# Performance work log

Measured on AMD Instinct MI355X. Metric: run time of the kernel, lower is better.

The kernel has to match this reference:

```python
import jax, jax.numpy as jnp
import numpy as np

N_NODES = 100000
N_EDGES = 600000
IN_FEATS = 128
OUT_FEATS = 128
BN_EPS = 1e-5


def setup_inputs() -> dict:
    key = jax.random.key(0)
    ks = jax.random.split(key, 8)
    x = jax.random.normal(ks[0], (N_NODES, IN_FEATS), dtype=jnp.float32)
    edge_index = jax.random.randint(ks[1], (2, N_EDGES), 0, N_NODES, dtype=jnp.int64)
    # GCNConv linear weight (no bias in lin), bias added after aggregation
    W = jax.random.normal(ks[2], (IN_FEATS, OUT_FEATS), dtype=jnp.float32) / np.sqrt(IN_FEATS)
    b = jax.random.normal(ks[3], (OUT_FEATS,), dtype=jnp.float32) * 0.01
    # BatchNorm affine params
    gamma = jnp.ones((OUT_FEATS,), dtype=jnp.float32)
    beta = jnp.zeros((OUT_FEATS,), dtype=jnp.float32)
    # residual Linear: y = x @ W_res + b_res (W_res stored [in, out])
    W_res = jax.random.normal(ks[4], (IN_FEATS, OUT_FEATS), dtype=jnp.float32) / np.sqrt(IN_FEATS)
    b_res = jax.random.normal(ks[5], (OUT_FEATS,), dtype=jnp.float32) * 0.01
    return {"x": x, "edge_index": edge_index, "W": W, "b": b,
            "gamma": gamma, "beta": beta, "W_res": W_res, "b_res": b_res}


def _gcn_forward(x, edge_index, W, b, gamma, beta, W_res, b_res):
    n = x.shape[0]
    # --- GCNConv (PyG defaults): add self-loops, symmetric normalization ---
    loops = jnp.arange(n, dtype=edge_index.dtype)
    row = jnp.concatenate([edge_index[0], loops])  # source nodes
    col = jnp.concatenate([edge_index[1], loops])  # destination nodes
    deg = jax.ops.segment_sum(jnp.ones_like(col, dtype=x.dtype), col, num_segments=n)
    dinv = jax.lax.rsqrt(deg)  # deg >= 1 thanks to self-loops
    norm = dinv[row] * dinv[col]  # [E+N]
    h = x @ W  # [N, out]
    msg = h[row] * norm[:, None]  # gather + scale, [E+N, out]
    agg = jax.ops.segment_sum(msg, col, num_segments=n) + b  # scatter-add + bias
    # --- ReLU + BatchNorm (training mode, biased variance) ---
    r = jax.nn.relu(agg)
    mean = jnp.mean(r, axis=0)
    var = jnp.mean(jnp.square(r - mean), axis=0)
    bn = gamma * (r - mean) * jax.lax.rsqrt(var + BN_EPS) + beta
    # --- residual dense path ---
    res = x @ W_res + b_res
    return bn + res


def reference(x, edge_index, W, b, gamma, beta, W_res, b_res):
    return _gcn_forward(x, edge_index, W, b, gamma, beta, W_res, b_res)
```

## Files before the change

kernel.cpp:

```cpp
#include <hip/hip_runtime.h>

#define NN 100000
#define NE 600000
#define F  128
#define BN_EPS 1e-5f


__global__ void k_detect(const unsigned* __restrict__ ei, int* __restrict__ flag)
{
    __shared__ int any;
    if (threadIdx.x == 0) any = 0;
    __syncthreads();
    unsigned v = ei[2 * threadIdx.x + 1];
    if (v != 0u) atomicOr(&any, 1);
    __syncthreads();
    if (threadIdx.x == 0) *flag = (any == 0) ? 1 : 0;
}

__global__ void k_init(int* __restrict__ cnt, float* __restrict__ colsum, float* __restrict__ colsq)
{
    int i = blockIdx.x * 256 + threadIdx.x;
    if (i <= NN) cnt[i] = 0;
    if (i < F) { colsum[i] = 0.f; colsq[i] = 0.f; }
}

__global__ void k_count(const void* __restrict__ ei, const int* __restrict__ flag, int* __restrict__ cnt)
{
    int e = blockIdx.x * 256 + threadIdx.x;
    if (e >= NE) return;
    int col;
    if (*flag) col = (int)((const long long*)ei)[NE + e];
    else       col = ((const int*)ei)[NE + e];
    atomicAdd(&cnt[col], 1);
}

__global__ void k_dinv(const int* __restrict__ cnt, float* __restrict__ dinv)
{
    int i = blockIdx.x * 256 + threadIdx.x;
    if (i < NN) {
        float d = (float)(cnt[i] + 1);
        float r = rsqrtf(d);
        r = r * (1.5f - 0.5f * d * r * r);
        dinv[i] = r;
    }
}

__global__ void k_bsum(const int* __restrict__ cnt, int* __restrict__ bsum)
{
    __shared__ int s[256];
    int b = blockIdx.x, t = threadIdx.x;
    int i = b * 256 + t;
    s[t] = (i <= NN) ? cnt[i] : 0;
    __syncthreads();
    for (int o = 128; o > 0; o >>= 1) {
        if (t < o) s[t] += s[t + o];
        __syncthreads();
    }
    if (t == 0) bsum[b] = s[0];
}

__global__ void k_bscan(const int* __restrict__ bsum, int* __restrict__ bbase)
{
    __shared__ int s[512];
    int t = threadIdx.x;
    int v = (t < 391) ? bsum[t] : 0;
    s[t] = v;
    __syncthreads();
    for (int o = 1; o < 512; o <<= 1) {
        int tmp = (t >= o) ? s[t - o] : 0;
        __syncthreads();
        s[t] += tmp;
        __syncthreads();
    }
    if (t < 391) bbase[t] = s[t] - v;
}

__global__ void k_offsets(const int* __restrict__ cnt, const int* __restrict__ bbase,
                          int* __restrict__ off, int* __restrict__ cur)
{
    __shared__ int s[256];
    int b = blockIdx.x, t = threadIdx.x;
    int i = b * 256 + t;
    int v = (i <= NN) ? cnt[i] : 0;
    s[t] = v;
    __syncthreads();
    for (int o = 1; o < 256; o <<= 1) {
        int tmp = (t >= o) ? s[t - o] : 0;
        __syncthreads();
        s[t] += tmp;
        __syncthreads();
    }
    int excl = s[t] - v + bbase[b];
    if (i <= NN) {
        off[i] = excl;
        if (i < NN) cur[i] = excl;
    }
}

__global__ void k_place(const void* __restrict__ ei, const int* __restrict__ flag,
                        int* __restrict__ cur, int* __restrict__ csr)
{
    int e = blockIdx.x * 256 + threadIdx.x;
    if (e >= NE) return;
    int row, col;
    if (*flag) {
        row = (int)((const long long*)ei)[e];
        col = (int)((const long long*)ei)[NE + e];
    } else {
        row = ((const int*)ei)[e];
        col = ((const int*)ei)[NE + e];
    }
    int slot = atomicAdd(&cur[col], 1);
    csr[slot] = row;
}

__global__ __launch_bounds__(256) void k_agg(const float* __restrict__ x, const float* __restrict__ dinv,
                                             const int* __restrict__ off, const int* __restrict__ csr,
                                             float* __restrict__ aggx)
{
    int g = threadIdx.x >> 5;
    int lane = threadIdx.x & 31;
    int node = blockIdx.x * 8 + g;
    if (node >= NN) return;
    float di = dinv[node];
    float4 v = ((const float4*)(x + (size_t)node * F))[lane];
    float4 acc;
    acc.x = v.x * di; acc.y = v.y * di; acc.z = v.z * di; acc.w = v.w * di;
    int e0 = off[node], e1 = off[node + 1];
    for (int e = e0; e < e1; ++e) {
        int row = csr[e];
        float s = dinv[row];
        float4 u = ((const float4*)(x + (size_t)row * F))[lane];
        acc.x = fmaf(u.x, s, acc.x);
        acc.y = fmaf(u.y, s, acc.y);
        acc.z = fmaf(u.z, s, acc.z);
        acc.w = fmaf(u.w, s, acc.w);
    }
    float4 o;
    o.x = acc.x * di; o.y = acc.y * di; o.z = acc.z * di; o.w = acc.w * di;
    ((float4*)(aggx + (size_t)node * F))[lane] = o;
}

__global__ __launch_bounds__(256, 2) void k_gemm(
    float* __restrict__ A, const float* __restrict__ X,
    const float* __restrict__ W, const float* __restrict__ Wr,
    const float* __restrict__ bias, const float* __restrict__ biasr,
    float* __restrict__ res_out, float* __restrict__ colsum, float* __restrict__ colsq)
{
    __shared__ float At[64][F];
    __shared__ float Xt[64][F];
    __shared__ float Wa[16][F];
    __shared__ float Wb[16][F];

    const int tid = threadIdx.x;
    const int tx = tid & 31;
    const int ty = tid >> 5;
    const int r0 = blockIdx.x * 64;

#pragma unroll
    for (int it = 0; it < 8; ++it) {
        int idx = tid + it * 256;
        int row = idx >> 5;
        int k4 = (idx & 31) << 2;
        int gr = r0 + row;
        float4 va = make_float4(0.f, 0.f, 0.f, 0.f);
        float4 vx = va;
        if (gr < NN) {
            va = *(const float4*)(A + (size_t)gr * F + k4);
            vx = *(const float4*)(X + (size_t)gr * F + k4);
        }
        *(float4*)(&At[row][k4]) = va;
        *(float4*)(&Xt[row][k4]) = vx;
    }

    float acc1[8][4], acc2[8][4];
#pragma unroll
    for (int i = 0; i < 8; ++i)
#pragma unroll
        for (int j = 0; j < 4; ++j) { acc1[i][j] = 0.f; acc2[i][j] = 0.f; }

    for (int c = 0; c < 8; ++c) {
        __syncthreads();
#pragma unroll
        for (int it = 0; it < 2; ++it) {
            int idx = tid + it * 256;
            int kr = idx >> 5;
            int kc = (idx & 31) << 2;
            *(float4*)(&Wa[kr][kc]) = *(const float4*)(W  + (c * 16 + kr) * F + kc);
            *(float4*)(&Wb[kr][kc]) = *(const float4*)(Wr + (c * 16 + kr) * F + kc);
        }
        __syncthreads();
#pragma unroll
        for (int k0 = 0; k0 < 16; k0 += 4) {
            float w1[4][4], w2[4][4];
#pragma unroll
            for (int kk = 0; kk < 4; ++kk) {
                float4 t1 = *(const float4*)(&Wa[k0 + kk][tx * 4]);
                float4 t2 = *(const float4*)(&Wb[k0 + kk][tx * 4]);
                w1[kk][0] = t1.x; w1[kk][1] = t1.y; w1[kk][2] = t1.z; w1[kk][3] = t1.w;
                w2[kk][0] = t2.x; w2[kk][1] = t2.y; w2[kk][2] = t2.z; w2[kk][3] = t2.w;
            }
#pragma unroll
            for (int i = 0; i < 8; ++i) {
                float4 a4 = *(const float4*)(&At[ty * 8 + i][c * 16 + k0]);
                float4 x4 = *(const float4*)(&Xt[ty * 8 + i][c * 16 + k0]);
                float av[4] = {a4.x, a4.y, a4.z, a4.w};
                float xv[4] = {x4.x, x4.y, x4.z, x4.w};
#pragma unroll
                for (int kk = 0; kk < 4; ++kk)
#pragma unroll
                    for (int j = 0; j < 4; ++j) {
                        acc1[i][j] = fmaf(av[kk], w1[kk][j], acc1[i][j]);
                        acc2[i][j] = fmaf(xv[kk], w2[kk][j], acc2[i][j]);
                    }
            }
        }
    }

    __syncthreads();
    float* s_sum = &Wa[0][0];
    float* s_sq  = &Wa[0][0] + 128;
    if (tid < 128) { s_sum[tid] = 0.f; s_sq[tid] = 0.f; }
    __syncthreads();

    float4 bv  = *(const float4*)(bias  + tx * 4);
    float4 brv = *(const float4*)(biasr + tx * 4);
    float bb[4]  = {bv.x, bv.y, bv.z, bv.w};
    float bb2[4] = {brv.x, brv.y, brv.z, brv.w};
    float ls[4] = {0.f, 0.f, 0.f, 0.f};
    float lq[4] = {0.f, 0.f, 0.f, 0.f};
#pragma unroll
    for (int i = 0; i < 8; ++i) {
        int gr = r0 + ty * 8 + i;
        if (gr < NN) {
            float r_[4], rs[4];
#pragma unroll
            for (int j = 0; j < 4; ++j) {
                float t = acc1[i][j] + bb[j];
                float r = fmaxf(t, 0.f);
                r_[j] = r;
                ls[j] += r;
                lq[j] = fmaf(r, r, lq[j]);
                rs[j] = acc2[i][j] + bb2[j];
            }
            *(float4*)(A + (size_t)gr * F + tx * 4)      = make_float4(r_[0], r_[1], r_[2], r_[3]);
            *(float4*)(res_out + (size_t)gr * F + tx * 4) = make_float4(rs[0], rs[1], rs[2], rs[3]);
        }
    }
#pragma unroll
    for (int j = 0; j < 4; ++j) {
        atomicAdd(&s_sum[tx * 4 + j], ls[j]);
        atomicAdd(&s_sq[tx * 4 + j], lq[j]);
    }
    __syncthreads();
    if (tid < 128) {
        atomicAdd(&colsum[tid], s_sum[tid]);
        atomicAdd(&colsq[tid], s_sq[tid]);
    }
}

__global__ void k_stats(const float* __restrict__ colsum, const float* __restrict__ colsq,
                        const float* __restrict__ gamma, const float* __restrict__ beta,
                        float* __restrict__ scale, float* __restrict__ shift)
{
    int c = threadIdx.x;
    if (c < F) {
        float inv_n = 1.0f / (float)NN;
        float mean = colsum[c] * inv_n;
        float ex2  = colsq[c] * inv_n;
        float var  = fmaxf(ex2 - mean * mean, 0.f);
        float d = var + BN_EPS;
        float is = rsqrtf(d);
        is = is * (1.5f - 0.5f * d * is * is);
        float sc = gamma[c] * is;
        scale[c] = sc;
        shift[c] = beta[c] - sc * mean;
    }
}

__global__ __launch_bounds__(256) void k_final(const float* __restrict__ r,
                                               const float* __restrict__ scale,
                                               const float* __restrict__ shift,
                                               float* __restrict__ out)
{
    int idx = blockIdx.x * 256 + threadIdx.x;
    int c4 = idx & 31;
    float4 rv = ((const float4*)r)[idx];
    float4 ov = ((float4*)out)[idx];
    float4 sv = ((const float4*)scale)[c4];
    float4 hv = ((const float4*)shift)[c4];
    float4 o;
    o.x = fmaf(rv.x, sv.x, hv.x) + ov.x;
    o.y = fmaf(rv.y, sv.y, hv.y) + ov.y;
    o.z = fmaf(rv.z, sv.z, hv.z) + ov.z;
    o.w = fmaf(rv.w, sv.w, hv.w) + ov.w;
    ((float4*)out)[idx] = o;
}

extern "C" void kernel_launch(void* const* d_in, const int* in_sizes, int n_in,
                              void* d_out, int out_size, void* d_ws, size_t ws_size,
                              hipStream_t stream)
{
    (void)in_sizes; (void)n_in; (void)out_size; (void)ws_size;
    const float* x     = (const float*)d_in[0];
    const void*  ei    = d_in[1];
    const float* W     = (const float*)d_in[2];
    const float* b     = (const float*)d_in[3];
    const float* gamma = (const float*)d_in[4];
    const float* beta  = (const float*)d_in[5];
    const float* Wres  = (const float*)d_in[6];
    const float* bres  = (const float*)d_in[7];
    float* out = (float*)d_out;

    char* w = (char*)d_ws;
    float* aggx   = (float*)(w + 0);
    int*   cnt    = (int*)  (w + 51200000);
    float* dinv   = (float*)(w + 51600128);
    int*   off    = (int*)  (w + 52000256);
    int*   cur    = (int*)  (w + 52400384);
    int*   csr    = (int*)  (w + 52800512);
    int*   bsum   = (int*)  (w + 55200512);
    int*   bbase  = (int*)  (w + 55202176);
    float* colsum = (float*)(w + 55203840);
    float* colsq  = (float*)(w + 55204352);
    float* scale  = (float*)(w + 55204864);
    float* shift  = (float*)(w + 55205376);
    int*   flag   = (int*)  (w + 55205888);

    const int G_INIT = 392;
    const int G_E    = (NE + 255) / 256;
    const int G_N    = 391;
    const int G_AGG  = 12500;
    const int G_GEMM = (NN + 63) / 64;
    const int G_FIN  = (NN * F / 4) / 256;

    k_detect <<<1, 256, 0, stream>>>((const unsigned*)ei, flag);
    k_init   <<<G_INIT, 256, 0, stream>>>(cnt, colsum, colsq);
    k_count  <<<G_E, 256, 0, stream>>>(ei, flag, cnt);
    k_dinv   <<<G_N, 256, 0, stream>>>(cnt, dinv);
    k_bsum   <<<G_N, 256, 0, stream>>>(cnt, bsum);
    k_bscan  <<<1, 512, 0, stream>>>(bsum, bbase);
    k_offsets<<<G_N, 256, 0, stream>>>(cnt, bbase, off, cur);
    k_place  <<<G_E, 256, 0, stream>>>(ei, flag, cur, csr);
    k_agg    <<<G_AGG, 256, 0, stream>>>(x, dinv, off, csr, aggx);
    k_gemm   <<<G_GEMM, 256, 0, stream>>>(aggx, x, W, Wres, b, bres, out, colsum, colsq);
    k_stats  <<<1, 128, 0, stream>>>(colsum, colsq, gamma, beta, scale, shift);
    k_final  <<<G_FIN, 256, 0, stream>>>(aggx, scale, shift, out);
}
```

Before: 382.5 us.

## Split dual GEMM into per-matrix tiles, widen aggregation wavefront, fuse dinv into offsets

The fused dual GEMM, which held both the A and X tiles in shared memory, becomes one kernel launched on a 2-wide grid. Each block computes either the conv path or the residual path with 128-row, 32-wide K tiles. This cuts shared memory per block and allows more resident blocks. The aggregation kernel now uses one 64-lane wavefront per node with float2 loads and an edge loop unrolled by two, and the separate dinv kernel is folded into k_offsets. The trade-off is that the residual path re-reads x in a separate block and the aggregation uses narrower per-lane loads.

```diff
diff --git a/kernel.cpp b/kernel.cpp
--- a/kernel.cpp
+++ b/kernel.cpp
@@ -4,7 +4,8 @@
 #define NE 600000
 #define F  128
 #define BN_EPS 1e-5f
-
+#define TM 128
+#define TK 32
 
 __global__ void k_detect(const unsigned* __restrict__ ei, int* __restrict__ flag)
 {
@@ -34,17 +35,6 @@
     atomicAdd(&cnt[col], 1);
 }
 
-__global__ void k_dinv(const int* __restrict__ cnt, float* __restrict__ dinv)
-{
-    int i = blockIdx.x * 256 + threadIdx.x;
-    if (i < NN) {
-        float d = (float)(cnt[i] + 1);
-        float r = rsqrtf(d);
-        r = r * (1.5f - 0.5f * d * r * r);
-        dinv[i] = r;
-    }
-}
-
 __global__ void k_bsum(const int* __restrict__ cnt, int* __restrict__ bsum)
 {
     __shared__ int s[256];
@@ -76,7 +66,8 @@
 }
 
 __global__ void k_offsets(const int* __restrict__ cnt, const int* __restrict__ bbase,
-                          int* __restrict__ off, int* __restrict__ cur)
+                          int* __restrict__ off, int* __restrict__ cur,
+                          float* __restrict__ dinv)
 {
     __shared__ int s[256];
     int b = blockIdx.x, t = threadIdx.x;
@@ -93,7 +84,13 @@
     int excl = s[t] - v + bbase[b];
     if (i <= NN) {
         off[i] = excl;
-        if (i < NN) cur[i] = excl;
+        if (i < NN) {
+            cur[i] = excl;
+            float d = (float)(v + 1);
+            float r = rsqrtf(d);
+            r = r * (1.5f - 0.5f * d * r * r);
+            dinv[i] = r;
+        }
     }
 }
 
@@ -118,144 +115,145 @@
                                              const int* __restrict__ off, const int* __restrict__ csr,
                                              float* __restrict__ aggx)
 {
-    int g = threadIdx.x >> 5;
-    int lane = threadIdx.x & 31;
-    int node = blockIdx.x * 8 + g;
+    int node = blockIdx.x * 4 + (threadIdx.x >> 6);
+    int lane = threadIdx.x & 63;
     if (node >= NN) return;
     float di = dinv[node];
-    float4 v = ((const float4*)(x + (size_t)node * F))[lane];
-    float4 acc;
-    acc.x = v.x * di; acc.y = v.y * di; acc.z = v.z * di; acc.w = v.w * di;
-    int e0 = off[node], e1 = off[node + 1];
-    for (int e = e0; e < e1; ++e) {
-        int row = csr[e];
-        float s = dinv[row];
-        float4 u = ((const float4*)(x + (size_t)row * F))[lane];
-        acc.x = fmaf(u.x, s, acc.x);
-        acc.y = fmaf(u.y, s, acc.y);
-        acc.z = fmaf(u.z, s, acc.z);
-        acc.w = fmaf(u.w, s, acc.w);
-    }
-    float4 o;
-    o.x = acc.x * di; o.y = acc.y * di; o.z = acc.z * di; o.w = acc.w * di;
-    ((float4*)(aggx + (size_t)node * F))[lane] = o;
-}
-
-__global__ __launch_bounds__(256, 2) void k_gemm(
+    float2 v = ((const float2*)(x + (size_t)node * F))[lane];
+    float ax = v.x * di, ay = v.y * di;
+    int e = off[node], e1 = off[node + 1];
+    for (; e + 1 < e1; e += 2) {
+        int r0 = csr[e], r1 = csr[e + 1];
+        float s0 = dinv[r0], s1 = dinv[r1];
+        float2 u0 = ((const float2*)(x + (size_t)r0 * F))[lane];
+        float2 u1 = ((const float2*)(x + (size_t)r1 * F))[lane];
+        ax = fmaf(u0.x, s0, ax); ay = fmaf(u0.y, s0, ay);
+        ax = fmaf(u1.x, s1, ax); ay = fmaf(u1.y, s1, ay);
+    }
+    if (e < e1) {
+        int r = csr[e]; float s = dinv[r];
+        float2 u = ((const float2*)(x + (size_t)r * F))[lane];
+        ax = fmaf(u.x, s, ax); ay = fmaf(u.y, s, ay);
+    }
+    float2 o; o.x = ax * di; o.y = ay * di;
+    ((float2*)(aggx + (size_t)node * F))[lane] = o;
+}
+
+__global__ __launch_bounds__(256, 4) void k_gemm2(
     float* __restrict__ A, const float* __restrict__ X,
     const float* __restrict__ W, const float* __restrict__ Wr,
     const float* __restrict__ bias, const float* __restrict__ biasr,
-    float* __restrict__ res_out, float* __restrict__ colsum, float* __restrict__ colsq)
-{
-    __shared__ float At[64][F];
-    __shared__ float Xt[64][F];
-    __shared__ float Wa[16][F];
-    __shared__ float Wb[16][F];
+    float* __restrict__ out, float* __restrict__ colsum, float* __restrict__ colsq)
+{
+    __shared__ float At[TM][TK];
+    __shared__ float Wt[TK][F];
 
     const int tid = threadIdx.x;
     const int tx = tid & 31;
     const int ty = tid >> 5;
-    const int r0 = blockIdx.x * 64;
-
-#pragma unroll
-    for (int it = 0; it < 8; ++it) {
-        int idx = tid + it * 256;
-        int row = idx >> 5;
-        int k4 = (idx & 31) << 2;
-        int gr = r0 + row;
-        float4 va = make_float4(0.f, 0.f, 0.f, 0.f);
-        float4 vx = va;
-        if (gr < NN) {
-            va = *(const float4*)(A + (size_t)gr * F + k4);
-            vx = *(const float4*)(X + (size_t)gr * F + k4);
-        }
-        *(float4*)(&At[row][k4]) = va;
-        *(float4*)(&Xt[row][k4]) = vx;
-    }
-
-    float acc1[8][4], acc2[8][4];
-#pragma unroll
-    for (int i = 0; i < 8; ++i)
-#pragma unroll
-        for (int j = 0; j < 4; ++j) { acc1[i][j] = 0.f; acc2[i][j] = 0.f; }
-
-    for (int c = 0; c < 8; ++c) {
-        __syncthreads();
-#pragma unroll
-        for (int it = 0; it < 2; ++it) {
+    const int type = blockIdx.y;
+    const int r0 = blockIdx.x * TM;
+    const float* __restrict__ src = type ? X : (const float*)A;
+    const float* __restrict__ wm  = type ? Wr : W;
+
+    float4 acc[16];
+#pragma unroll
+    for (int i = 0; i < 16; ++i) acc[i] = make_float4(0.f, 0.f, 0.f, 0.f);
+
+    for (int kc = 0; kc < 4; ++kc) {
+        __syncthreads();
+#pragma unroll
+        for (int it = 0; it < 4; ++it) {
+            int idx = tid + it * 256;
+            int row = idx >> 3;
+            int slot = idx & 7;
+            int gr = r0 + row;
+            float4 v = make_float4(0.f, 0.f, 0.f, 0.f);
+            if (gr < NN) v = *(const float4*)(src + (size_t)gr * F + kc * TK + slot * 4);
+            *(float4*)(&At[row][slot * 4]) = v;
+        }
+#pragma unroll
+        for (int it = 0; it < 4; ++it) {
             int idx = tid + it * 256;
             int kr = idx >> 5;
-            int kc = (idx & 31) << 2;
-            *(float4*)(&Wa[kr][kc]) = *(const float4*)(W  + (c * 16 + kr) * F + kc);
-            *(float4*)(&Wb[kr][kc]) = *(const float4*)(Wr + (c * 16 + kr) * F + kc);
-        }
-        __syncthreads();
-#pragma unroll
-        for (int k0 = 0; k0 < 16; k0 += 4) {
-            float w1[4][4], w2[4][4];
-#pragma unroll
-            for (int kk = 0; kk < 4; ++kk) {
-                float4 t1 = *(const float4*)(&Wa[k0 + kk][tx * 4]);
-                float4 t2 = *(const float4*)(&Wb[k0 + kk][tx * 4]);
-                w1[kk][0] = t1.x; w1[kk][1] = t1.y; w1[kk][2] = t1.z; w1[kk][3] = t1.w;
-                w2[kk][0] = t2.x; w2[kk][1] = t2.y; w2[kk][2] = t2.z; w2[kk][3] = t2.w;
+            int jc = (idx & 31) << 2;
+            *(float4*)(&Wt[kr][jc]) = *(const float4*)(wm + (size_t)(kc * TK + kr) * F + jc);
+        }
+        __syncthreads();
+#pragma unroll
+        for (int kq = 0; kq < 8; ++kq) {
+            float4 w0 = *(const float4*)(&Wt[kq * 4 + 0][tx * 4]);
+            float4 w1 = *(const float4*)(&Wt[kq * 4 + 1][tx * 4]);
+            float4 w2 = *(const float4*)(&Wt[kq * 4 + 2][tx * 4]);
+            float4 w3 = *(const float4*)(&Wt[kq * 4 + 3][tx * 4]);
+#pragma unroll
+            for (int i = 0; i < 16; ++i) {
+                float4 a = *(const float4*)(&At[ty * 16 + i][kq * 4]);
+                acc[i].x = fmaf(a.x, w0.x, acc[i].x);
+                acc[i].y = fmaf(a.x, w0.y, acc[i].y);
+                acc[i].z = fmaf(a.x, w0.z, acc[i].z);
+                acc[i].w = fmaf(a.x, w0.w, acc[i].w);
+                acc[i].x = fmaf(a.y, w1.x, acc[i].x);
+                acc[i].y = fmaf(a.y, w1.y, acc[i].y);
+                acc[i].z = fmaf(a.y, w1.z, acc[i].z);
+                acc[i].w = fmaf(a.y, w1.w, acc[i].w);
+                acc[i].x = fmaf(a.z, w2.x, acc[i].x);
+                acc[i].y = fmaf(a.z, w2.y, acc[i].y);
+                acc[i].z = fmaf(a.z, w2.z, acc[i].z);
+                acc[i].w = fmaf(a.z, w2.w, acc[i].w);
+                acc[i].x = fmaf(a.w, w3.x, acc[i].x);
+                acc[i].y = fmaf(a.w, w3.y, acc[i].y);
+                acc[i].z = fmaf(a.w, w3.z, acc[i].z);
+                acc[i].w = fmaf(a.w, w3.w, acc[i].w);
             }
-#pragma unroll
-            for (int i = 0; i < 8; ++i) {
-                float4 a4 = *(const float4*)(&At[ty * 8 + i][c * 16 + k0]);
-                float4 x4 = *(const float4*)(&Xt[ty * 8 + i][c * 16 + k0]);
-                float av[4] = {a4.x, a4.y, a4.z, a4.w};
-                float xv[4] = {x4.x, x4.y, x4.z, x4.w};
-#pragma unroll
-                for (int kk = 0; kk < 4; ++kk)
-#pragma unroll
-                    for (int j = 0; j < 4; ++j) {
-                        acc1[i][j] = fmaf(av[kk], w1[kk][j], acc1[i][j]);
-                        acc2[i][j] = fmaf(xv[kk], w2[kk][j], acc2[i][j]);
-                    }
+        }
+    }
+    __syncthreads();
+
+    if (type == 0) {
+        float* ssum = &Wt[0][0];
+        float* ssq  = &Wt[0][0] + F;
+        if (tid < F) { ssum[tid] = 0.f; ssq[tid] = 0.f; }
+        __syncthreads();
+        float4 bv = *(const float4*)(bias + tx * 4);
+        float ls[4] = {0.f, 0.f, 0.f, 0.f};
+        float lq[4] = {0.f, 0.f, 0.f, 0.f};
+#pragma unroll
+        for (int i = 0; i < 16; ++i) {
+            int gr = r0 + ty * 16 + i;
+            if (gr < NN) {
+                float r0_ = fmaxf(acc[i].x + bv.x, 0.f);
+                float r1_ = fmaxf(acc[i].y + bv.y, 0.f);
+                float r2_ = fmaxf(acc[i].z + bv.z, 0.f);
+                float r3_ = fmaxf(acc[i].w + bv.w, 0.f);
+                ls[0] += r0_; lq[0] = fmaf(r0_, r0_, lq[0]);
+                ls[1] += r1_; lq[1] = fmaf(r1_, r1_, lq[1]);
+                ls[2] += r2_; lq[2] = fmaf(r2_, r2_, lq[2]);
+                ls[3] += r3_; lq[3] = fmaf(r3_, r3_, lq[3]);
+                *(float4*)(A + (size_t)gr * F + tx * 4) = make_float4(r0_, r1_, r2_, r3_);
             }
         }
-    }
-
-    __syncthreads();
-    float* s_sum = &Wa[0][0];
-    float* s_sq  = &Wa[0][0] + 128;
-    if (tid < 128) { s_sum[tid] = 0.f; s_sq[tid] = 0.f; }
-    __syncthreads();
-
-    float4 bv  = *(const float4*)(bias  + tx * 4);
-    float4 brv = *(const float4*)(biasr + tx * 4);
-    float bb[4]  = {bv.x, bv.y, bv.z, bv.w};
-    float bb2[4] = {brv.x, brv.y, brv.z, brv.w};
-    float ls[4] = {0.f, 0.f, 0.f, 0.f};
-    float lq[4] = {0.f, 0.f, 0.f, 0.f};
-#pragma unroll
-    for (int i = 0; i < 8; ++i) {
-        int gr = r0 + ty * 8 + i;
-        if (gr < NN) {
-            float r_[4], rs[4];
-#pragma unroll
-            for (int j = 0; j < 4; ++j) {
-                float t = acc1[i][j] + bb[j];
-                float r = fmaxf(t, 0.f);
-                r_[j] = r;
-                ls[j] += r;
-                lq[j] = fmaf(r, r, lq[j]);
-                rs[j] = acc2[i][j] + bb2[j];
+#pragma unroll
+        for (int j = 0; j < 4; ++j) {
+            atomicAdd(&ssum[tx * 4 + j], ls[j]);
+            atomicAdd(&ssq[tx * 4 + j], lq[j]);
+        }
+        __syncthreads();
+        if (tid < F) {
+            atomicAdd(&colsum[tid], ssum[tid]);
+            atomicAdd(&colsq[tid], ssq[tid]);
+        }
+    } else {
+        float4 bv = *(const float4*)(biasr + tx * 4);
+#pragma unroll
+        for (int i = 0; i < 16; ++i) {
+            int gr = r0 + ty * 16 + i;
+            if (gr < NN) {
+                *(float4*)(out + (size_t)gr * F + tx * 4) =
+                    make_float4(acc[i].x + bv.x, acc[i].y + bv.y,
+                                acc[i].z + bv.z, acc[i].w + bv.w);
             }
-            *(float4*)(A + (size_t)gr * F + tx * 4)      = make_float4(r_[0], r_[1], r_[2], r_[3]);
-            *(float4*)(res_out + (size_t)gr * F + tx * 4) = make_float4(rs[0], rs[1], rs[2], rs[3]);
-        }
-    }
-#pragma unroll
-    for (int j = 0; j < 4; ++j) {
-        atomicAdd(&s_sum[tx * 4 + j], ls[j]);
-        atomicAdd(&s_sq[tx * 4 + j], lq[j]);
-    }
-    __syncthreads();
-    if (tid < 128) {
-        atomicAdd(&colsum[tid], s_sum[tid]);
-        atomicAdd(&colsq[tid], s_sq[tid]);
+        }
     }
 }
 
@@ -330,20 +328,19 @@
     const int G_INIT = 392;
     const int G_E    = (NE + 255) / 256;
     const int G_N    = 391;
-    const int G_AGG  = 12500;
-    const int G_GEMM = (NN + 63) / 64;
+    const int G_AGG  = (NN + 3) / 4;
+    const dim3 G_GEMM((NN + TM - 1) / TM, 2);
     const int G_FIN  = (NN * F / 4) / 256;
 
     k_detect <<<1, 256, 0, stream>>>((const unsigned*)ei, flag);
     k_init   <<<G_INIT, 256, 0, stream>>>(cnt, colsum, colsq);
     k_count  <<<G_E, 256, 0, stream>>>(ei, flag, cnt);
-    k_dinv   <<<G_N, 256, 0, stream>>>(cnt, dinv);
     k_bsum   <<<G_N, 256, 0, stream>>>(cnt, bsum);
     k_bscan  <<<1, 512, 0, stream>>>(bsum, bbase);
-    k_offsets<<<G_N, 256, 0, stream>>>(cnt, bbase, off, cur);
+    k_offsets<<<G_N, 256, 0, stream>>>(cnt, bbase, off, cur, dinv);
     k_place  <<<G_E, 256, 0, stream>>>(ei, flag, cur, csr);
     k_agg    <<<G_AGG, 256, 0, stream>>>(x, dinv, off, csr, aggx);
-    k_gemm   <<<G_GEMM, 256, 0, stream>>>(aggx, x, W, Wres, b, bres, out, colsum, colsq);
+    k_gemm2  <<<G_GEMM, 256, 0, stream>>>(aggx, x, W, Wres, b, bres, out, colsum, colsq);
     k_stats  <<<1, 128, 0, stream>>>(colsum, colsq, gamma, beta, scale, shift);
     k_final  <<<G_FIN, 256, 0, stream>>>(aggx, scale, shift, out);
 }
```

Measured after the change: 468.2 us. 1.22x slower.
